# Performance work log

Measured on AMD Instinct MI355X. Metric: run time of the kernel, lower is better.

Reference implementation:

```python
import jax, jax.numpy as jnp
import numpy as np

E = 1152          # embed_dim (Qwen3-VL vision hidden_size)
H = 16            # num_heads
D = E // H        # head_dim = 72
SEG = 8           # number of frames / attention segments
HW = 32           # each frame is 32x32 patches -> seg_len = 1024
L = HW * HW
S = SEG * L       # total tokens = 8192


def _make_rotary(S):
    # VisionRotaryEmbedding(dim=head_dim//2): inv_freq over arange(0, 36, 2)/36 -> 18 freqs
    half = D // 2  # 36
    inv_freq = 1.0 / (10000.0 ** (jnp.arange(0, half, 2, dtype=jnp.float32) / half))  # (18,)
    # 2D (h,w) position ids within each 32x32 frame, tiled across frames
    hpos = jnp.tile(jnp.repeat(jnp.arange(HW, dtype=jnp.float32), HW), SEG)  # (S,)
    wpos = jnp.tile(jnp.tile(jnp.arange(HW, dtype=jnp.float32), HW), SEG)    # (S,)
    fh = hpos[:, None] * inv_freq[None, :]   # (S, 18)
    fw = wpos[:, None] * inv_freq[None, :]   # (S, 18)
    freqs = jnp.concatenate([fh, fw], axis=-1)       # (S, 36)
    emb = jnp.concatenate([freqs, freqs], axis=-1)   # (S, 72) = head_dim
    return jnp.cos(emb), jnp.sin(emb)


def setup_inputs() -> dict:
    key = jax.random.key(0)
    k = jax.random.split(key, 6)
    std = 1.0 / np.sqrt(E)
    cos, sin = _make_rotary(S)
    return {
        "x": jax.random.normal(k[0], (S, E), jnp.float32),
        "cos": cos,
        "sin": sin,
        "qkv_w": jax.random.normal(k[1], (3 * E, E), jnp.float32) * std,
        "qkv_b": jax.random.normal(k[2], (3 * E,), jnp.float32) * 0.02,
        "proj_w": jax.random.normal(k[3], (E, E), jnp.float32) * std,
        "proj_b": jax.random.normal(k[4], (E,), jnp.float32) * 0.02,
        "cu_seqlens": jnp.arange(SEG + 1, dtype=jnp.int32) * L,
    }


def _rope(t, cos, sin):
    # t: (S, H, D); cos/sin: (S, D) broadcast over heads (matches cos.unsqueeze(1))
    half = t.shape[-1] // 2
    t1, t2 = t[..., :half], t[..., half:]
    rot = jnp.concatenate([-t2, t1], axis=-1)
    return t * cos[:, None, :] + rot * sin[:, None, :]


def reference(x, cos, sin, qkv_w, qkv_b, proj_w, proj_b, cu_seqlens):
    S_, E_ = x.shape
    qkv = x @ qkv_w.T + qkv_b                     # (S, 3E)
    q, k, v = jnp.split(qkv, 3, axis=-1)
    q = _rope(q.reshape(S_, H, D), cos, sin)
    k = _rope(k.reshape(S_, H, D), cos, sin)
    v = v.reshape(S_, H, D)
    # Equal-length segments (one per frame): block-diagonal attention via reshape,
    # honoring cu_seqlens structure without materializing an (S, S) mask.
    nseg = cu_seqlens.shape[0] - 1
    Lseg = S_ // nseg
    qs = q.reshape(nseg, Lseg, H, D)
    ks = k.reshape(nseg, Lseg, H, D)
    vs = v.reshape(nseg, Lseg, H, D)
    scale = 1.0 / np.sqrt(D)
    logits = jnp.einsum('gqhd,gkhd->ghqk', qs, ks) * scale   # (nseg, H, L, L)
    attn = jax.nn.softmax(logits, axis=-1)
    out = jnp.einsum('ghqk,gkhd->gqhd', attn, vs).reshape(S_, E_)
    return out @ proj_w.T + proj_b
```

## Files before the change

### kernel.cpp

```cpp
#include <hip/hip_runtime.h>
#include <hip/hip_bf16.h>
#include <stdint.h>

#define SEGN 8
#define LSEG 1024
#define SS   8192
#define EE   1152
#define HH   16
#define DD   72
#define DP   96
#define E3   3456
#define E3P  3584

typedef __attribute__((ext_vector_type(8)))  __bf16 bf16x8;
typedef __attribute__((ext_vector_type(4)))  float  f32x4;
typedef __attribute__((ext_vector_type(16))) float  f32x16;
typedef __attribute__((ext_vector_type(4)))  unsigned int u32x4;

__device__ __forceinline__ short f2b(float x) {
  __hip_bfloat16 h = __float2bfloat16(x);
  return __builtin_bit_cast(short, h);
}
__device__ __forceinline__ float b2f(short x) {
  return __bfloat162float(__builtin_bit_cast(__hip_bfloat16, x));
}
__device__ __forceinline__ unsigned int pk2(float x, float y) {
  return (unsigned int)(unsigned short)f2b(x) |
         ((unsigned int)(unsigned short)f2b(y) << 16);
}
__device__ __forceinline__ void gload16(const void* g, void* l) {
  __builtin_amdgcn_global_load_lds(
      (const __attribute__((address_space(1))) unsigned int*)g,
      (__attribute__((address_space(3))) unsigned int*)l, 16, 0, 0);
}

#define BAR() __builtin_amdgcn_s_barrier()
#define LGKM0() do { asm volatile("s_waitcnt lgkmcnt(0)" ::: "memory"); \
                     __builtin_amdgcn_sched_barrier(0); } while (0)

__global__ void k_cvt(const float* __restrict__ in, short* __restrict__ out, int n4) {
  int i = blockIdx.x * blockDim.x + threadIdx.x;
  int stride = gridDim.x * blockDim.x;
  for (; i < n4; i += stride) {
    float4 v = reinterpret_cast<const float4*>(in)[i];
    short4 o;
    o.x = f2b(v.x); o.y = f2b(v.y); o.z = f2b(v.z); o.w = f2b(v.w);
    reinterpret_cast<short4*>(out)[i] = o;
  }
}

__global__ __launch_bounds__(512, 2) void k_gemm256(
    const short* __restrict__ A, const short* __restrict__ B,
    const float* __restrict__ bias, short* __restrict__ C,
    int M, int K, int Nreal)
{
  __shared__ __align__(16) short As[3][256 * 32];
  __shared__ __align__(16) short Bs[3][256 * 32];
  const int t = threadIdx.x;
  const int lane = t & 63, wave = t >> 6;
  const int r16 = lane & 15, kg = lane >> 4;
  const int wm = wave >> 2, wn = wave & 3;
  const int m0 = blockIdx.x * 256, n0 = blockIdx.y * 256;
  const int NT = K >> 5;

  const int D0 = t * 16, D1 = (t + 512) * 16;
  const int L0 = D0 ^ (((D0 >> 7) & 3) << 4);
  const int L1 = D1 ^ (((D1 >> 7) & 3) << 4);
  const int sr0 = L0 >> 6, sc0 = (L0 & 63) >> 1;
  const int sr1 = L1 >> 6, sc1 = (L1 & 63) >> 1;
  const short* pA0 = A + (size_t)(m0 + sr0) * K + sc0;
  const short* pA1 = A + (size_t)(m0 + sr1) * K + sc1;
  const short* pB0 = B + (size_t)(n0 + sr0) * K + sc0;
  const short* pB1 = B + (size_t)(n0 + sr1) * K + sc1;

  const int xorv = ((r16 >> 1) & 3) << 4;
  const int abase = (wm * 128 + r16) * 64 + ((kg * 16) ^ xorv);
  const int bbase = (wn * 64 + r16) * 64 + ((kg * 16) ^ xorv);

  f32x4 acc[8][4] = {};

  gload16(pA0, (char*)As[0] + D0); gload16(pA1, (char*)As[0] + D1);
  gload16(pB0, (char*)Bs[0] + D0); gload16(pB1, (char*)Bs[0] + D1);
  gload16(pA0 + 32, (char*)As[1] + D0); gload16(pA1 + 32, (char*)As[1] + D1);
  gload16(pB0 + 32, (char*)Bs[1] + D0); gload16(pB1 + 32, (char*)Bs[1] + D1);
  asm volatile("s_waitcnt vmcnt(4)" ::: "memory");
  BAR();

  int cur = 0;
  for (int kt = 0; kt < NT; ++kt) {
    int nb = cur + 2; if (nb >= 3) nb -= 3;
    const char* bufA = (const char*)As[cur];
    const char* bufB = (const char*)Bs[cur];
    const bool pf = (kt + 2 < NT);
    const int koff = (kt + 2) * 32;

    bf16x8 a_[4], b_[4];
#pragma unroll
    for (int m = 0; m < 4; ++m)
      a_[m] = *(const bf16x8*)(bufA + abase + m * 1024);
#pragma unroll
    for (int n = 0; n < 4; ++n)
      b_[n] = *(const bf16x8*)(bufB + bbase + n * 1024);
    if (pf) {
      gload16(pA0 + koff, (char*)As[nb] + D0);
      gload16(pA1 + koff, (char*)As[nb] + D1);
    }
    BAR();
    LGKM0();
    __builtin_amdgcn_s_setprio(1);
#pragma unroll
    for (int m = 0; m < 4; ++m)
#pragma unroll
      for (int n = 0; n < 4; ++n)
        acc[m][n] = __builtin_amdgcn_mfma_f32_16x16x32_bf16(a_[m], b_[n], acc[m][n], 0, 0, 0);
    __builtin_amdgcn_s_setprio(0);
    BAR();

    bf16x8 a2_[4];
#pragma unroll
    for (int m = 0; m < 4; ++m)
      a2_[m] = *(const bf16x8*)(bufA + abase + (m + 4) * 1024);
    if (pf) {
      gload16(pB0 + koff, (char*)Bs[nb] + D0);
      gload16(pB1 + koff, (char*)Bs[nb] + D1);
    }
    BAR();
    LGKM0();
    __builtin_amdgcn_s_setprio(1);
#pragma unroll
    for (int m = 0; m < 4; ++m)
#pragma unroll
      for (int n = 0; n < 4; ++n)
        acc[m + 4][n] = __builtin_amdgcn_mfma_f32_16x16x32_bf16(a2_[m], b_[n], acc[m + 4][n], 0, 0, 0);
    __builtin_amdgcn_s_setprio(0);
    if (pf) { asm volatile("s_waitcnt vmcnt(4)" ::: "memory"); }
    else    { asm volatile("s_waitcnt vmcnt(0)" ::: "memory"); }
    BAR();

    cur = cur + 1; if (cur >= 3) cur = 0;
  }

#pragma unroll
  for (int n = 0; n < 4; ++n) {
    int col = n0 + wn * 64 + n * 16 + r16;
    if (col < Nreal) {
      float bv = bias[col];
#pragma unroll
      for (int m = 0; m < 8; ++m)
#pragma unroll
        for (int r = 0; r < 4; ++r) {
          int row = m0 + wm * 128 + m * 16 + kg * 4 + r;
          C[(size_t)row * Nreal + col] = f2b(acc[m][n][r] + bv);
        }
    }
  }
}

__global__ __launch_bounds__(256) void k_gemm_bt_f32(
    const short* __restrict__ A, const short* __restrict__ B,
    const float* __restrict__ bias, float* __restrict__ Cout,
    int M, int N, int K)
{
  __shared__ __align__(16) short As[128 * 64];
  __shared__ __align__(16) short Bs[128 * 64];
  const int t = threadIdx.x;
  const int lane = t & 63, wave = t >> 6;
  const int r16 = lane & 15, kg = lane >> 4;
  const int m0 = blockIdx.x * 128, n0 = blockIdx.y * 128;
  const int wr = (wave >> 1) * 64, wc = (wave & 1) * 64;

  f32x4 acc[4][4] = {};

  for (int k0 = 0; k0 < K; k0 += 64) {
    __syncthreads();
#pragma unroll
    for (int i = 0; i < 4; ++i) {
      int c0 = wave * 64 + i * 256;
      int c = c0 + lane;
      int row = c >> 3, col = (c & 7) * 8;
      gload16(A + (m0 + row) * K + k0 + col, (char*)As + c0 * 16);
      gload16(B + (n0 + row) * K + k0 + col, (char*)Bs + c0 * 16);
    }
    __syncthreads();
#pragma unroll
    for (int kk = 0; kk < 2; ++kk) {
      bf16x8 a[4], b[4];
#pragma unroll
      for (int m = 0; m < 4; ++m)
        a[m] = *(const bf16x8*)&As[(wr + m * 16 + r16) * 64 + kk * 32 + kg * 8];
#pragma unroll
      for (int n = 0; n < 4; ++n)
        b[n] = *(const bf16x8*)&Bs[(wc + n * 16 + r16) * 64 + kk * 32 + kg * 8];
#pragma unroll
      for (int m = 0; m < 4; ++m)
#pragma unroll
        for (int n = 0; n < 4; ++n)
          acc[m][n] = __builtin_amdgcn_mfma_f32_16x16x32_bf16(a[m], b[n], acc[m][n], 0, 0, 0);
    }
  }

#pragma unroll
  for (int n = 0; n < 4; ++n) {
    int col = n0 + wc + n * 16 + r16;
    float bv = bias[col];
#pragma unroll
    for (int m = 0; m < 4; ++m) {
#pragma unroll
      for (int r = 0; r < 4; ++r) {
        int row = m0 + wr + m * 16 + kg * 4 + r;
        Cout[row * N + col] = acc[m][n][r] + bv;
      }
    }
  }
}

__global__ __launch_bounds__(256) void k_rope(
    const short* __restrict__ qkv, const float* __restrict__ cosb, const float* __restrict__ sinb,
    short* __restrict__ Qg, short* __restrict__ Kg, short* __restrict__ Vg)
{
  __shared__ short vt[72][64];
  const int b = blockIdx.x;
  const int seg = b >> 8, head = (b >> 4) & 15, pb = b & 15;
  const int pos0 = pb * 64;
  const int t = threadIdx.x;
  const int sh = seg * 16 + head;
  const float qscale = 0.17002540410995343f;

#pragma unroll
  for (int i = 0; i < 24; ++i) {
    int e = t + i * 256;
    int p = e / 96, d = e % 96;
    int s = seg * 1024 + pos0 + p;
    int ob = (sh * 1024 + pos0 + p) * 96 + d;
    short qo = 0, ko = 0;
    if (d < 72) {
      int base = s * E3 + head * 72;
      float c = cosb[s * 72 + d], sn = sinb[s * 72 + d];
      int d2 = d < 36 ? d + 36 : d - 36;
      float sgn = d < 36 ? -1.f : 1.f;
      float q1 = b2f(qkv[base + d]),        q2 = b2f(qkv[base + d2]);
      float k1 = b2f(qkv[base + 1152 + d]), k2 = b2f(qkv[base + 1152 + d2]);
      qo = f2b((q1 * c + sgn * q2 * sn) * qscale);
      ko = f2b(k1 * c + sgn * k2 * sn);
    }
    Qg[ob] = qo;
    Kg[ob] = ko;
  }
  for (int i = 0; i < 18; ++i) {
    int e = t + i * 256;
    int p = e / 72, d = e % 72;
    int s = seg * 1024 + pos0 + p;
    vt[d][p] = qkv[s * E3 + 2304 + head * 72 + d];
  }
  __syncthreads();
#pragma unroll
  for (int i = 0; i < 24; ++i) {
    int e = t + i * 256;
    int d = e >> 6, p = e & 63;
    short v;
    if (d < 72)       v = vt[d][p];
    else if (d == 72) v = (short)0x3F80;
    else              v = 0;
    Vg[(sh * 96 + d) * 1024 + pos0 + p] = v;
  }
}

#define KSS 104
#define VTS 72
__global__ __launch_bounds__(256, 3) void k_attn(
    const short* __restrict__ Qg, const short* __restrict__ Kg, const short* __restrict__ Vg,
    short* __restrict__ Og)
{
  __shared__ __align__(16) short Ks[64 * KSS];
  __shared__ __align__(16) short VT[96 * VTS];
  const int p_ = blockIdx.x;
  const int xcd = p_ & 7, rest = p_ >> 3;
  const int qb = rest & 7, shi = rest >> 3;
  const int sh = xcd * 16 + shi;
  const int seg = sh >> 4, head = sh & 15;
  const int t = threadIdx.x, lane = t & 63, wave = t >> 6;
  const int l31 = lane & 31, hi = lane >> 5;
  const int q0 = qb * 128 + wave * 32;

  bf16x8 qf[6];
  {
    const short* qp = Qg + ((size_t)(sh * 1024 + q0 + l31)) * 96 + hi * 8;
#pragma unroll
    for (int dm = 0; dm < 6; ++dm) qf[dm] = *(const bf16x8*)(qp + dm * 16);
  }

  const short* kbase = Kg + (size_t)sh * 1024 * 96;
  const short* vbase = Vg + (size_t)sh * 96 * 1024;
  int koff[4], voff[4];
#pragma unroll
  for (int i = 0; i < 4; ++i) {
    int c = t + i * 256;
    int kr = c / 13, kc8 = c - kr * 13;
    koff[i] = kr * 96 + ((kc8 == 12) ? 0 : kc8 * 8);
    int vr = c / 9, vc8 = c - vr * 9;
    voff[i] = vr * 1024 + ((vc8 == 8) ? 0 : vc8 * 8);
  }

  f32x16 acc0 = {}, acc1 = {}, acc2 = {};
  float Mrun = -1e30f;

  for (int kt = 0; kt < 16; ++kt) {
    __syncthreads();
    {
      const short* kp = kbase + kt * 64 * 96;
      const short* vp = vbase + kt * 64;
#pragma unroll
      for (int i = 0; i < 3; ++i) {
        gload16(kp + koff[i], (char*)Ks + (t + i * 256) * 16);
        gload16(vp + voff[i], (char*)VT + (t + i * 256) * 16);
      }
      if (t < 64) gload16(kp + koff[3], (char*)Ks + (t + 768) * 16);
      if (t < 96) gload16(vp + voff[3], (char*)VT + (t + 768) * 16);
    }
    __syncthreads();

    f32x16 s0 = {}, s1 = {};
#pragma unroll
    for (int dm = 0; dm < 6; ++dm) {
      bf16x8 kf0 = *(const bf16x8*)&Ks[l31 * KSS + dm * 16 + hi * 8];
      bf16x8 kf1 = *(const bf16x8*)&Ks[(32 + l31) * KSS + dm * 16 + hi * 8];
      s0 = __builtin_amdgcn_mfma_f32_32x32x16_bf16(kf0, qf[dm], s0, 0, 0, 0);
      s1 = __builtin_amdgcn_mfma_f32_32x32x16_bf16(kf1, qf[dm], s1, 0, 0, 0);
    }

    float pmax = s0[0];
#pragma unroll
    for (int r = 1; r < 16; ++r) pmax = fmaxf(pmax, s0[r]);
#pragma unroll
    for (int r = 0; r < 16; ++r) pmax = fmaxf(pmax, s1[r]);
    pmax = fmaxf(pmax, __shfl_xor(pmax, 32));

    if (__any(pmax > Mrun + 8.0f)) {
      float mn = fmaxf(Mrun, pmax);
      float corr = exp2f(Mrun - mn);
      Mrun = mn;
#pragma unroll
      for (int r = 0; r < 16; ++r) {
        int qr = (r & 3) + 8 * (r >> 2) + 4 * hi;
        float cr = __shfl(corr, qr);
        acc0[r] *= cr; acc1[r] *= cr; acc2[r] *= cr;
      }
    }

    unsigned int pk0[8], pk1[8];
#pragma unroll
    for (int b = 0; b < 4; ++b)
#pragma unroll
      for (int i = 0; i < 2; ++i) {
        pk0[b * 2 + i] = pk2(exp2f(s0[b * 4 + 2 * i] - Mrun), exp2f(s0[b * 4 + 2 * i + 1] - Mrun));
        pk1[b * 2 + i] = pk2(exp2f(s1[b * 4 + 2 * i] - Mrun), exp2f(s1[b * 4 + 2 * i + 1] - Mrun));
      }

#pragma unroll
    for (int ks = 0; ks < 4; ++ks) {
      const int k1 = ks & 1;
      unsigned int A0, A1, B0, B1;
      if (ks < 2) { A0 = pk0[4 * k1]; A1 = pk0[4 * k1 + 1]; B0 = pk0[4 * k1 + 2]; B1 = pk0[4 * k1 + 3]; }
      else        { A0 = pk1[4 * k1]; A1 = pk1[4 * k1 + 1]; B0 = pk1[4 * k1 + 2]; B1 = pk1[4 * k1 + 3]; }
      unsigned int SA0 = __shfl_xor((int)A0, 32), SA1 = __shfl_xor((int)A1, 32);
      unsigned int SB0 = __shfl_xor((int)B0, 32), SB1 = __shfl_xor((int)B1, 32);
      u32x4 wv;
      wv.x = hi ? SB0 : A0;
      wv.y = hi ? SB1 : A1;
      wv.z = hi ? B0 : SA0;
      wv.w = hi ? B1 : SA1;
      bf16x8 af = __builtin_bit_cast(bf16x8, wv);
      bf16x8 vf0 = *(const bf16x8*)&VT[l31 * VTS + ks * 16 + hi * 8];
      bf16x8 vf1 = *(const bf16x8*)&VT[(32 + l31) * VTS + ks * 16 + hi * 8];
      bf16x8 vf2 = *(const bf16x8*)&VT[(64 + l31) * VTS + ks * 16 + hi * 8];
      acc0 = __builtin_amdgcn_mfma_f32_32x32x16_bf16(af, vf0, acc0, 0, 0, 0);
      acc1 = __builtin_amdgcn_mfma_f32_32x32x16_bf16(af, vf1, acc1, 0, 0, 0);
      acc2 = __builtin_amdgcn_mfma_f32_32x32x16_bf16(af, vf2, acc2, 0, 0, 0);
    }
  }

#pragma unroll
  for (int r = 0; r < 16; ++r) {
    float l = __shfl(acc2[r], (lane & 32) | 8);
    float inv = 1.0f / l;
    int q = q0 + (r & 3) + 8 * (r >> 2) + 4 * hi;
    size_t base = (size_t)(seg * 1024 + q) * 1152 + head * 72;
    Og[base + l31]      = f2b(acc0[r] * inv);
    Og[base + 32 + l31] = f2b(acc1[r] * inv);
    if (l31 < 8) Og[base + 64 + l31] = f2b(acc2[r] * inv);
  }
}

extern "C" void kernel_launch(void* const* d_in, const int* in_sizes, int n_in,
                              void* d_out, int out_size, void* d_ws, size_t ws_size,
                              hipStream_t stream) {
  (void)in_sizes; (void)n_in; (void)out_size; (void)ws_size;
  const float* x      = (const float*)d_in[0];
  const float* cosb   = (const float*)d_in[1];
  const float* sinb   = (const float*)d_in[2];
  const float* qkv_w  = (const float*)d_in[3];
  const float* qkv_b  = (const float*)d_in[4];
  const float* proj_w = (const float*)d_in[5];
  const float* proj_b = (const float*)d_in[6];

  char* ws = (char*)d_ws;
  size_t o = 0;
  short* xb  = (short*)(ws + o); o += (size_t)SS * EE * 2;
  short* qwb = (short*)(ws + o); o += (size_t)E3P * EE * 2;
  short* pwb = (short*)(ws + o); o += (size_t)EE * EE * 2;
  short* qkv = (short*)(ws + o); o += (size_t)SS * E3 * 2;
  short* Qg  = (short*)(ws + o); o += (size_t)SEGN * HH * LSEG * DP * 2;
  short* Kg  = (short*)(ws + o); o += (size_t)SEGN * HH * LSEG * DP * 2;
  short* Vg  = (short*)(ws + o); o += (size_t)SEGN * HH * DP * LSEG * 2;
  short* og  = xb;

  k_cvt<<<2048, 256, 0, stream>>>(x, xb, SS * EE / 4);
  k_cvt<<<1024, 256, 0, stream>>>(qkv_w, qwb, E3 * EE / 4);
  k_cvt<<<512, 256, 0, stream>>>(proj_w, pwb, EE * EE / 4);

  dim3 g1(SS / 256, E3P / 256);
  k_gemm256<<<g1, 512, 0, stream>>>(xb, qwb, qkv_b, qkv, SS, EE, E3);

  k_rope<<<SEGN * HH * 16, 256, 0, stream>>>(qkv, cosb, sinb, Qg, Kg, Vg);

  k_attn<<<SEGN * HH * 8, 256, 0, stream>>>(Qg, Kg, Vg, og);

  dim3 g2(SS / 128, EE / 128);
  k_gemm_bt_f32<<<g2, 256, 0, stream>>>(og, pwb, proj_b, (float*)d_out, SS, EE, EE);
}
```

Baseline: 284.9 us.

## Restructure 256-tile GEMM to BK=64 double buffer, reuse it for output projection

The 256x256 GEMM moves from a triple-buffered K=32 pipeline to a double-buffered K=64 pipeline. Each 64-row subtile gets an 8-way XOR-swizzled LDS layout, and loads are staged in four phases per iteration. It also adds an XCD-aware block-index swizzle and templates the output type, so the output projection now uses this kernel with the weight padded to 1280 rows instead of the simpler 128x128 kernel. The change aims to cut barrier overhead per K step and improve L2 locality. The risk is the padded proj rows: pwb rows 1152..1279 are left unconverted in the workspace (though the column guard masks their output), and the proj GEMM has few blocks (160).

```diff
diff --git a/kernel.cpp b/kernel.cpp
--- a/kernel.cpp
+++ b/kernel.cpp
@@ -11,6 +11,7 @@
 #define DP   96
 #define E3   3456
 #define E3P  3584
+#define EEP  1280
 
 typedef __attribute__((ext_vector_type(8)))  __bf16 bf16x8;
 typedef __attribute__((ext_vector_type(4)))  float  f32x4;
@@ -49,96 +50,145 @@
   }
 }
 
+template <int OUT_BF16>
 __global__ __launch_bounds__(512, 2) void k_gemm256(
     const short* __restrict__ A, const short* __restrict__ B,
-    const float* __restrict__ bias, short* __restrict__ C,
-    int M, int K, int Nreal)
+    const float* __restrict__ bias, void* __restrict__ Cout,
+    int K, int Nreal)
 {
-  __shared__ __align__(16) short As[3][256 * 32];
-  __shared__ __align__(16) short Bs[3][256 * 32];
+  __shared__ __align__(16) short Als[2][4][64 * 64];
+  __shared__ __align__(16) short Bls[2][4][64 * 64];
   const int t = threadIdx.x;
   const int lane = t & 63, wave = t >> 6;
   const int r16 = lane & 15, kg = lane >> 4;
   const int wm = wave >> 2, wn = wave & 3;
-  const int m0 = blockIdx.x * 256, n0 = blockIdx.y * 256;
-  const int NT = K >> 5;
-
-  const int D0 = t * 16, D1 = (t + 512) * 16;
-  const int L0 = D0 ^ (((D0 >> 7) & 3) << 4);
-  const int L1 = D1 ^ (((D1 >> 7) & 3) << 4);
-  const int sr0 = L0 >> 6, sc0 = (L0 & 63) >> 1;
-  const int sr1 = L1 >> 6, sc1 = (L1 & 63) >> 1;
-  const short* pA0 = A + (size_t)(m0 + sr0) * K + sc0;
-  const short* pA1 = A + (size_t)(m0 + sr1) * K + sc1;
-  const short* pB0 = B + (size_t)(n0 + sr0) * K + sc0;
-  const short* pB1 = B + (size_t)(n0 + sr1) * K + sc1;
-
-  const int xorv = ((r16 >> 1) & 3) << 4;
-  const int abase = (wm * 128 + r16) * 64 + ((kg * 16) ^ xorv);
-  const int bbase = (wn * 64 + r16) * 64 + ((kg * 16) ^ xorv);
+
+  const int nwg = gridDim.x * gridDim.y;
+  const int fid = blockIdx.y * gridDim.x + blockIdx.x;
+  const int cpx = nwg >> 3;
+  const int swz = (fid & 7) * cpx + (fid >> 3);
+  const int m0 = (swz % gridDim.x) * 256, n0 = (swz / gridDim.x) * 256;
+  const int NT = K >> 6;
+
+  const int D = t * 16;
+  const int L = D ^ (((D >> 7) & 7) << 4);
+  const int srow = L >> 7, scol = (L & 127) >> 1;
+  const short* pa = A + (size_t)(m0 + srow) * K + scol;
+  const short* pb = B + (size_t)(n0 + srow) * K + scol;
+  const int K64 = K * 64;
+
+#define STAGE_A(bf, h, kt_) do { \
+    gload16(pa + (h) * K64 + (kt_) * 64, (char*)Als[bf][h] + D); \
+    gload16(pa + ((h) + 2) * K64 + (kt_) * 64, (char*)Als[bf][(h) + 2] + D); } while (0)
+#define STAGE_B(bf, h, kt_) do { \
+    gload16(pb + (h) * K64 + (kt_) * 64, (char*)Bls[bf][h] + D); \
+    gload16(pb + ((h) + 2) * K64 + (kt_) * 64, (char*)Bls[bf][(h) + 2] + D); } while (0)
+
+  const int cA0 = (kg * 16) ^ ((r16 & 7) << 4);
+  const int cA1 = (64 + kg * 16) ^ ((r16 & 7) << 4);
 
   f32x4 acc[8][4] = {};
 
-  gload16(pA0, (char*)As[0] + D0); gload16(pA1, (char*)As[0] + D1);
-  gload16(pB0, (char*)Bs[0] + D0); gload16(pB1, (char*)Bs[0] + D1);
-  gload16(pA0 + 32, (char*)As[1] + D0); gload16(pA1 + 32, (char*)As[1] + D1);
-  gload16(pB0 + 32, (char*)Bs[1] + D0); gload16(pB1 + 32, (char*)Bs[1] + D1);
+  STAGE_A(0, 0, 0); STAGE_B(0, 0, 0);
+  STAGE_A(0, 1, 0); STAGE_B(0, 1, 0);
+  STAGE_A(1, 0, 1); STAGE_B(1, 0, 1);
   asm volatile("s_waitcnt vmcnt(4)" ::: "memory");
   BAR();
 
-  int cur = 0;
   for (int kt = 0; kt < NT; ++kt) {
-    int nb = cur + 2; if (nb >= 3) nb -= 3;
-    const char* bufA = (const char*)As[cur];
-    const char* bufB = (const char*)Bs[cur];
-    const bool pf = (kt + 2 < NT);
-    const int koff = (kt + 2) * 32;
-
-    bf16x8 a_[4], b_[4];
-#pragma unroll
-    for (int m = 0; m < 4; ++m)
-      a_[m] = *(const bf16x8*)(bufA + abase + m * 1024);
-#pragma unroll
-    for (int n = 0; n < 4; ++n)
-      b_[n] = *(const bf16x8*)(bufB + bbase + n * 1024);
-    if (pf) {
-      gload16(pA0 + koff, (char*)As[nb] + D0);
-      gload16(pA1 + koff, (char*)As[nb] + D1);
-    }
+    const int bsel = kt & 1, bn1 = bsel ^ 1;
+    const bool s1 = (kt + 1 < NT), s2 = (kt + 2 < NT);
+    const char* aq0 = (const char*)Als[bsel][2 * wm];
+    const char* aq1 = (const char*)Als[bsel][2 * wm + 1];
+    const char* bq  = (const char*)Bls[bsel][wn];
+
+    bf16x8 a_[2][2], b_[4][2];
+
+#pragma unroll
+    for (int mi = 0; mi < 2; ++mi) {
+      a_[mi][0] = *(const bf16x8*)(aq0 + (mi * 16 + r16) * 128 + cA0);
+      a_[mi][1] = *(const bf16x8*)(aq0 + (mi * 16 + r16) * 128 + cA1);
+    }
+#pragma unroll
+    for (int n = 0; n < 4; ++n) {
+      b_[n][0] = *(const bf16x8*)(bq + (n * 16 + r16) * 128 + cA0);
+      b_[n][1] = *(const bf16x8*)(bq + (n * 16 + r16) * 128 + cA1);
+    }
+    if (s1) STAGE_A(bn1, 1, kt + 1);
     BAR();
     LGKM0();
     __builtin_amdgcn_s_setprio(1);
 #pragma unroll
-    for (int m = 0; m < 4; ++m)
-#pragma unroll
-      for (int n = 0; n < 4; ++n)
-        acc[m][n] = __builtin_amdgcn_mfma_f32_16x16x32_bf16(a_[m], b_[n], acc[m][n], 0, 0, 0);
+    for (int mi = 0; mi < 2; ++mi)
+#pragma unroll
+      for (int n = 0; n < 4; ++n) {
+        acc[mi][n] = __builtin_amdgcn_mfma_f32_16x16x32_bf16(a_[mi][0], b_[n][0], acc[mi][n], 0, 0, 0);
+        acc[mi][n] = __builtin_amdgcn_mfma_f32_16x16x32_bf16(a_[mi][1], b_[n][1], acc[mi][n], 0, 0, 0);
+      }
     __builtin_amdgcn_s_setprio(0);
     BAR();
 
-    bf16x8 a2_[4];
-#pragma unroll
-    for (int m = 0; m < 4; ++m)
-      a2_[m] = *(const bf16x8*)(bufA + abase + (m + 4) * 1024);
-    if (pf) {
-      gload16(pB0 + koff, (char*)Bs[nb] + D0);
-      gload16(pB1 + koff, (char*)Bs[nb] + D1);
-    }
+#pragma unroll
+    for (int mi = 0; mi < 2; ++mi) {
+      a_[mi][0] = *(const bf16x8*)(aq0 + ((mi + 2) * 16 + r16) * 128 + cA0);
+      a_[mi][1] = *(const bf16x8*)(aq0 + ((mi + 2) * 16 + r16) * 128 + cA1);
+    }
+    if (s1) STAGE_B(bn1, 1, kt + 1);
     BAR();
     LGKM0();
     __builtin_amdgcn_s_setprio(1);
 #pragma unroll
-    for (int m = 0; m < 4; ++m)
-#pragma unroll
-      for (int n = 0; n < 4; ++n)
-        acc[m + 4][n] = __builtin_amdgcn_mfma_f32_16x16x32_bf16(a2_[m], b_[n], acc[m + 4][n], 0, 0, 0);
+    for (int mi = 0; mi < 2; ++mi)
+#pragma unroll
+      for (int n = 0; n < 4; ++n) {
+        acc[mi + 2][n] = __builtin_amdgcn_mfma_f32_16x16x32_bf16(a_[mi][0], b_[n][0], acc[mi + 2][n], 0, 0, 0);
+        acc[mi + 2][n] = __builtin_amdgcn_mfma_f32_16x16x32_bf16(a_[mi][1], b_[n][1], acc[mi + 2][n], 0, 0, 0);
+      }
     __builtin_amdgcn_s_setprio(0);
-    if (pf) { asm volatile("s_waitcnt vmcnt(4)" ::: "memory"); }
+    BAR();
+
+#pragma unroll
+    for (int mi = 0; mi < 2; ++mi) {
+      a_[mi][0] = *(const bf16x8*)(aq1 + (mi * 16 + r16) * 128 + cA0);
+      a_[mi][1] = *(const bf16x8*)(aq1 + (mi * 16 + r16) * 128 + cA1);
+    }
+    if (s2) STAGE_A(bsel, 0, kt + 2);
+    BAR();
+    LGKM0();
+    __builtin_amdgcn_s_setprio(1);
+#pragma unroll
+    for (int mi = 0; mi < 2; ++mi)
+#pragma unroll
+      for (int n = 0; n < 4; ++n) {
+        acc[mi + 4][n] = __builtin_amdgcn_mfma_f32_16x16x32_bf16(a_[mi][0], b_[n][0], acc[mi + 4][n], 0, 0, 0);
+        acc[mi + 4][n] = __builtin_amdgcn_mfma_f32_16x16x32_bf16(a_[mi][1], b_[n][1], acc[mi + 4][n], 0, 0, 0);
+      }
+    __builtin_amdgcn_s_setprio(0);
+    BAR();
+
+#pragma unroll
+    for (int mi = 0; mi < 2; ++mi) {
+      a_[mi][0] = *(const bf16x8*)(aq1 + ((mi + 2) * 16 + r16) * 128 + cA0);
+      a_[mi][1] = *(const bf16x8*)(aq1 + ((mi + 2) * 16 + r16) * 128 + cA1);
+    }
+    if (s2) STAGE_B(bsel, 0, kt + 2);
+    BAR();
+    LGKM0();
+    __builtin_amdgcn_s_setprio(1);
+#pragma unroll
+    for (int mi = 0; mi < 2; ++mi)
+#pragma unroll
+      for (int n = 0; n < 4; ++n) {
+        acc[mi + 6][n] = __builtin_amdgcn_mfma_f32_16x16x32_bf16(a_[mi][0], b_[n][0], acc[mi + 6][n], 0, 0, 0);
+        acc[mi + 6][n] = __builtin_amdgcn_mfma_f32_16x16x32_bf16(a_[mi][1], b_[n][1], acc[mi + 6][n], 0, 0, 0);
+      }
+    __builtin_amdgcn_s_setprio(0);
+    if (s2) { asm volatile("s_waitcnt vmcnt(4)" ::: "memory"); }
     else    { asm volatile("s_waitcnt vmcnt(0)" ::: "memory"); }
     BAR();
-
-    cur = cur + 1; if (cur >= 3) cur = 0;
-  }
+  }
+#undef STAGE_A
+#undef STAGE_B
 
 #pragma unroll
   for (int n = 0; n < 4; ++n) {
@@ -150,66 +200,10 @@
 #pragma unroll
         for (int r = 0; r < 4; ++r) {
           int row = m0 + wm * 128 + m * 16 + kg * 4 + r;
-          C[(size_t)row * Nreal + col] = f2b(acc[m][n][r] + bv);
+          float v = acc[m][n][r] + bv;
+          if (OUT_BF16) ((short*)Cout)[(size_t)row * Nreal + col] = f2b(v);
+          else          ((float*)Cout)[(size_t)row * Nreal + col] = v;
         }
-    }
-  }
-}
-
-__global__ __launch_bounds__(256) void k_gemm_bt_f32(
-    const short* __restrict__ A, const short* __restrict__ B,
-    const float* __restrict__ bias, float* __restrict__ Cout,
-    int M, int N, int K)
-{
-  __shared__ __align__(16) short As[128 * 64];
-  __shared__ __align__(16) short Bs[128 * 64];
-  const int t = threadIdx.x;
-  const int lane = t & 63, wave = t >> 6;
-  const int r16 = lane & 15, kg = lane >> 4;
-  const int m0 = blockIdx.x * 128, n0 = blockIdx.y * 128;
-  const int wr = (wave >> 1) * 64, wc = (wave & 1) * 64;
-
-  f32x4 acc[4][4] = {};
-
-  for (int k0 = 0; k0 < K; k0 += 64) {
-    __syncthreads();
-#pragma unroll
-    for (int i = 0; i < 4; ++i) {
-      int c0 = wave * 64 + i * 256;
-      int c = c0 + lane;
-      int row = c >> 3, col = (c & 7) * 8;
-      gload16(A + (m0 + row) * K + k0 + col, (char*)As + c0 * 16);
-      gload16(B + (n0 + row) * K + k0 + col, (char*)Bs + c0 * 16);
-    }
-    __syncthreads();
-#pragma unroll
-    for (int kk = 0; kk < 2; ++kk) {
-      bf16x8 a[4], b[4];
-#pragma unroll
-      for (int m = 0; m < 4; ++m)
-        a[m] = *(const bf16x8*)&As[(wr + m * 16 + r16) * 64 + kk * 32 + kg * 8];
-#pragma unroll
-      for (int n = 0; n < 4; ++n)
-        b[n] = *(const bf16x8*)&Bs[(wc + n * 16 + r16) * 64 + kk * 32 + kg * 8];
-#pragma unroll
-      for (int m = 0; m < 4; ++m)
-#pragma unroll
-        for (int n = 0; n < 4; ++n)
-          acc[m][n] = __builtin_amdgcn_mfma_f32_16x16x32_bf16(a[m], b[n], acc[m][n], 0, 0, 0);
-    }
-  }
-
-#pragma unroll
-  for (int n = 0; n < 4; ++n) {
-    int col = n0 + wc + n * 16 + r16;
-    float bv = bias[col];
-#pragma unroll
-    for (int m = 0; m < 4; ++m) {
-#pragma unroll
-      for (int r = 0; r < 4; ++r) {
-        int row = m0 + wr + m * 16 + kg * 4 + r;
-        Cout[row * N + col] = acc[m][n][r] + bv;
-      }
     }
   }
 }
@@ -407,7 +401,7 @@
   size_t o = 0;
   short* xb  = (short*)(ws + o); o += (size_t)SS * EE * 2;
   short* qwb = (short*)(ws + o); o += (size_t)E3P * EE * 2;
-  short* pwb = (short*)(ws + o); o += (size_t)EE * EE * 2;
+  short* pwb = (short*)(ws + o); o += (size_t)EEP * EE * 2;
   short* qkv = (short*)(ws + o); o += (size_t)SS * E3 * 2;
   short* Qg  = (short*)(ws + o); o += (size_t)SEGN * HH * LSEG * DP * 2;
   short* Kg  = (short*)(ws + o); o += (size_t)SEGN * HH * LSEG * DP * 2;
@@ -419,12 +413,12 @@
   k_cvt<<<512, 256, 0, stream>>>(proj_w, pwb, EE * EE / 4);
 
   dim3 g1(SS / 256, E3P / 256);
-  k_gemm256<<<g1, 512, 0, stream>>>(xb, qwb, qkv_b, qkv, SS, EE, E3);
+  k_gemm256<1><<<g1, 512, 0, stream>>>(xb, qwb, qkv_b, qkv, EE, E3);
 
   k_rope<<<SEGN * HH * 16, 256, 0, stream>>>(qkv, cosb, sinb, Qg, Kg, Vg);
 
   k_attn<<<SEGN * HH * 8, 256, 0, stream>>>(Qg, Kg, Vg, og);
 
-  dim3 g2(SS / 128, EE / 128);
-  k_gemm_bt_f32<<<g2, 256, 0, stream>>>(og, pwb, proj_b, (float*)d_out, SS, EE, EE);
-}
+  dim3 g2(SS / 256, EEP / 256);
+  k_gemm256<0><<<g2, 512, 0, stream>>>(og, pwb, proj_b, d_out, EE, EE);
+}
```

New measurement: 271.4 us. -4.7%, faster.
